# Kernel tuning notes

Measured on AMD Instinct MI355X. Metric: run time of the kernel, lower is better.

Reference implementation:

```python
import jax, jax.numpy as jnp
import numpy as np

TOTAL_TOKENS = 1_000_000   # total ragged flat values
EMB = 128                  # embedding_size
BATCH = 8192               # number of ragged rows (segments)


def setup_inputs() -> dict:
    key = jax.random.key(0)
    k1, k2, k3, k4, k5 = jax.random.split(key, 5)
    value = jax.random.normal(k1, (TOTAL_TOKENS, EMB), dtype=jnp.float32)
    key_emb = jax.random.normal(k2, (TOTAL_TOKENS, EMB), dtype=jnp.float32)
    segment_ids = jnp.sort(jax.random.randint(k3, (TOTAL_TOKENS,), 0, BATCH))
    fingerprint = jax.random.normal(k4, (EMB,), dtype=jnp.float32)
    w = jax.random.normal(k5, (EMB, EMB), dtype=jnp.float32) * 0.05
    return {"value": value, "key_emb": key_emb, "segment_ids": segment_ids,
            "fingerprint": fingerprint, "w": w}


def reference(value, key_emb, segment_ids, fingerprint, w):
    # Ragged branch: scores[i] = sum_k key[i,k] * w[k,k] * fingerprint[k]
    scale = jnp.sqrt(jnp.asarray(EMB, jnp.float32))
    diag_wf = jnp.diagonal(w) * fingerprint          # [E]
    scores = (key_emb @ diag_wf) / scale             # [T]
    # segment-wise (per ragged row) softmax
    smax = jax.ops.segment_max(scores, segment_ids, num_segments=BATCH)  # [B]
    ex = jnp.exp(scores - smax[segment_ids])                              # [T]
    denom = jax.ops.segment_sum(ex, segment_ids, num_segments=BATCH)     # [B]
    wts = ex / denom[segment_ids]                                         # [T]
    # weighted sum of concat([value, key], -1) over each ragged row
    feats = jnp.concatenate([value, key_emb], axis=-1)                    # [T, 2E]
    out = jax.ops.segment_sum(wts[:, None] * feats, segment_ids,
                              num_segments=BATCH)                         # [B, 2E]
    return out
```

## Files before the change

kernel.cpp:

```cpp
#include <hip/hip_runtime.h>
#include <cstdint>
#include <math.h>

#define EMB 128
#define CHUNK 64

__global__ void seg_starts_kernel(const int* __restrict__ seg, int T, int B,
                                  int* __restrict__ starts) {
    int b = blockIdx.x * blockDim.x + threadIdx.x;
    if (b > B) return;
    int lo = 0, hi = T;
    while (lo < hi) {
        int mid = (lo + hi) >> 1;
        if (seg[mid] < b) lo = mid + 1; else hi = mid;
    }
    starts[b] = lo;
}

__global__ __launch_bounds__(256, 4) void attn_kernel(
    const float* __restrict__ value, const float* __restrict__ key,
    const int* __restrict__ starts, const float* __restrict__ fingerprint,
    const float* __restrict__ w, float* __restrict__ out)
{
    __shared__ float key_lds[CHUNK * EMB];
    __shared__ float s_lds[CHUNK];
    __shared__ float e_lds[CHUNK];
    __shared__ float dwf_lds[EMB];
    __shared__ float red2[2];

    const int b   = blockIdx.x;
    const int tid = threadIdx.x;
    const int s0  = starts[b];
    const int s1  = starts[b + 1];
    const int len = s1 - s0;

    if (tid < EMB)
        dwf_lds[tid] = w[tid * EMB + tid] * fingerprint[tid] * 0.08838834764831845f;
    __syncthreads();

    const int lane = tid & 63;
    const int wv   = tid >> 6;
    const float dlo = dwf_lds[lane];
    const float dhi = dwf_lds[lane + 64];

    float acc   = 0.0f;
    float m     = -INFINITY;
    float denom = 0.0f;

    for (int o = 0; o < len; o += CHUNK) {
        const int cl = min(CHUNK, len - o);

        const float4* kbase = (const float4*)(key + (size_t)(s0 + o) * EMB);
        const int n4 = cl * (EMB / 4);
        for (int f = tid; f < n4; f += 256)
            ((float4*)key_lds)[f] = kbase[f];
        __syncthreads();

        for (int r = 0; r < CHUNK / 4; ++r) {
            int t = wv + 4 * r;
            if (t < cl) {
                float sc = key_lds[t * EMB + lane] * dlo
                         + key_lds[t * EMB + lane + 64] * dhi;
                #pragma unroll
                for (int off = 32; off; off >>= 1) sc += __shfl_xor(sc, off);
                if (lane == 0) s_lds[t] = sc;
            } else {
                if (lane == 0) s_lds[t] = -INFINITY;
            }
        }
        __syncthreads();

        const float m_old = m;
        if (wv == 0) {
            float s  = s_lds[lane];
            float mx = s;
            #pragma unroll
            for (int off = 32; off; off >>= 1) mx = fmaxf(mx, __shfl_xor(mx, off));
            float m_new = fmaxf(m_old, mx);
            float e = (s > -INFINITY) ? __expf(s - m_new) : 0.0f;
            e_lds[lane] = e;
            float ss = e;
            #pragma unroll
            for (int off = 32; off; off >>= 1) ss += __shfl_xor(ss, off);
            if (lane == 0) { red2[0] = m_new; red2[1] = ss; }
        }
        __syncthreads();
        const float m_new = red2[0];
        const float csum  = red2[1];
        const float alpha = (m_old > -INFINITY) ? __expf(m_old - m_new) : 0.0f;
        acc   = acc * alpha;
        denom = denom * alpha + csum;
        m     = m_new;

        if (tid < 128) {
            const float* vcol = value + (size_t)(s0 + o) * EMB + tid;
            #pragma unroll 4
            for (int t = 0; t < cl; ++t)
                acc = fmaf(e_lds[t], vcol[(size_t)t * EMB], acc);
        } else {
            const float* kcol = key_lds + (tid - 128);
            #pragma unroll 4
            for (int t = 0; t < cl; ++t)
                acc = fmaf(e_lds[t], kcol[t * EMB], acc);
        }
        __syncthreads();
    }

    const float r = (denom > 0.0f) ? acc / denom : 0.0f;
    out[(size_t)b * (2 * EMB) + tid] = r;
}

extern "C" void kernel_launch(void* const* d_in, const int* in_sizes, int n_in,
                              void* d_out, int out_size, void* d_ws, size_t ws_size,
                              hipStream_t stream) {
    const float* value = (const float*)d_in[0];
    const float* key   = (const float*)d_in[1];
    const int*   seg   = (const int*)d_in[2];
    const float* fp    = (const float*)d_in[3];
    const float* w     = (const float*)d_in[4];
    float* out = (float*)d_out;

    const int T = in_sizes[2];
    const int B = out_size / (2 * EMB);

    int* starts = (int*)d_ws;

    const int nb = (B + 1 + 255) / 256;
    seg_starts_kernel<<<nb, 256, 0, stream>>>(seg, T, B, starts);
    attn_kernel<<<B, 256, 0, stream>>>(value, key, starts, fp, w, out);
}
```

Before: 1.066 ms.

## Use direct global-to-LDS key loads with swizzle and vectorized row-parallel accumulation

Key chunks now go straight from global memory into LDS through global_load_lds, laid out with an XOR swizzle, and the chunk size drops to 32 with a higher occupancy hint. Scoring runs 8 lanes per row over float4 reads, every wave computes the softmax redundantly so one barrier and the shared e buffer go away, and the weighted sum is spread across waves and row halves as float4 accumulators. A final cross-wave reduction through LDS replaces the old per-column serial loops. The aim is to remove strided scalar global value loads and LDS bank conflicts. In exchange the kernel does more chunk iterations and a final reduction step, and clamped indices read extra rows whose weight is zero.

```diff
diff --git a/kernel.cpp b/kernel.cpp
--- a/kernel.cpp
+++ b/kernel.cpp
@@ -3,7 +3,7 @@
 #include <math.h>
 
 #define EMB 128
-#define CHUNK 64
+#define CHUNK 32
 
 __global__ void seg_starts_kernel(const int* __restrict__ seg, int T, int B,
                                   int* __restrict__ starts) {
@@ -17,19 +17,20 @@
     starts[b] = lo;
 }
 
-__global__ __launch_bounds__(256, 4) void attn_kernel(
+__global__ __launch_bounds__(256, 6) void attn_kernel(
     const float* __restrict__ value, const float* __restrict__ key,
     const int* __restrict__ starts, const float* __restrict__ fingerprint,
-    const float* __restrict__ w, float* __restrict__ out)
+    const float* __restrict__ w, float* __restrict__ out, int T)
 {
-    __shared__ float key_lds[CHUNK * EMB];
+    __shared__ __align__(16) float key_lds[CHUNK * EMB];
     __shared__ float s_lds[CHUNK];
-    __shared__ float e_lds[CHUNK];
-    __shared__ float dwf_lds[EMB];
-    __shared__ float red2[2];
+    __shared__ __align__(16) float dwf_lds[EMB];
 
-    const int b   = blockIdx.x;
-    const int tid = threadIdx.x;
+    const int b    = blockIdx.x;
+    const int tid  = threadIdx.x;
+    const int lane = tid & 63;
+    const int wv   = tid >> 6;
+
     const int s0  = starts[b];
     const int s1  = starts[b + 1];
     const int len = s1 - s0;
@@ -38,75 +39,116 @@
         dwf_lds[tid] = w[tid * EMB + tid] * fingerprint[tid] * 0.08838834764831845f;
     __syncthreads();
 
-    const int lane = tid & 63;
-    const int wv   = tid >> 6;
-    const float dlo = dwf_lds[lane];
-    const float dhi = dwf_lds[lane + 64];
+    const int g8   = lane >> 3;
+    const int j8   = lane & 7;
+    const int half = lane >> 5;
+    const int c4   = lane & 31;
 
-    float acc   = 0.0f;
-    float m     = -INFINITY;
-    float denom = 0.0f;
+    float4 dw[4];
+    #pragma unroll
+    for (int q = 0; q < 4; ++q)
+        dw[q] = *reinterpret_cast<const float4*>(&dwf_lds[j8 * 16 + q * 4]);
+
+    float4 vacc = make_float4(0.f, 0.f, 0.f, 0.f);
+    float4 kacc = make_float4(0.f, 0.f, 0.f, 0.f);
+    float m = -INFINITY, denom = 0.0f;
+
+    const char* key_b = (const char*)key;
 
     for (int o = 0; o < len; o += CHUNK) {
         const int cl = min(CHUNK, len - o);
 
-        const float4* kbase = (const float4*)(key + (size_t)(s0 + o) * EMB);
-        const int n4 = cl * (EMB / 4);
-        for (int f = tid; f < n4; f += 256)
-            ((float4*)key_lds)[f] = kbase[f];
-        __syncthreads();
-
-        for (int r = 0; r < CHUNK / 4; ++r) {
-            int t = wv + 4 * r;
-            if (t < cl) {
-                float sc = key_lds[t * EMB + lane] * dlo
-                         + key_lds[t * EMB + lane + 64] * dhi;
-                #pragma unroll
-                for (int off = 32; off; off >>= 1) sc += __shfl_xor(sc, off);
-                if (lane == 0) s_lds[t] = sc;
-            } else {
-                if (lane == 0) s_lds[t] = -INFINITY;
-            }
+        #pragma unroll
+        for (int i = 0; i < 4; ++i) {
+            const int q  = (wv << 2) + i;
+            const int r  = (q << 1) + half;
+            const int gr = min(s0 + o + r, T - 1);
+            const char* src = key_b + (size_t)gr * 512 + ((c4 ^ (r & 7)) << 4);
+            __builtin_amdgcn_global_load_lds(
+                (const __attribute__((address_space(1))) void*)src,
+                (__attribute__((address_space(3))) void*)(key_lds + (q << 8)),
+                16, 0, 0);
         }
         __syncthreads();
 
-        const float m_old = m;
-        if (wv == 0) {
-            float s  = s_lds[lane];
-            float mx = s;
-            #pragma unroll
-            for (int off = 32; off; off >>= 1) mx = fmaxf(mx, __shfl_xor(mx, off));
-            float m_new = fmaxf(m_old, mx);
-            float e = (s > -INFINITY) ? __expf(s - m_new) : 0.0f;
-            e_lds[lane] = e;
-            float ss = e;
-            #pragma unroll
-            for (int off = 32; off; off >>= 1) ss += __shfl_xor(ss, off);
-            if (lane == 0) { red2[0] = m_new; red2[1] = ss; }
+        {
+            const int t = (wv << 3) + g8;
+            float sc = 0.0f;
+            if (t < cl) {
+                const char* rowp = (const char*)key_lds + t * 512;
+                const int swz = (t & 7) << 4;
+                #pragma unroll
+                for (int q = 0; q < 4; ++q) {
+                    const float4 k = *reinterpret_cast<const float4*>(
+                        rowp + (((((j8 << 2) + q) << 4)) ^ swz));
+                    sc = fmaf(k.x, dw[q].x, sc);
+                    sc = fmaf(k.y, dw[q].y, sc);
+                    sc = fmaf(k.z, dw[q].z, sc);
+                    sc = fmaf(k.w, dw[q].w, sc);
+                }
+            }
+            sc += __shfl_xor(sc, 1);
+            sc += __shfl_xor(sc, 2);
+            sc += __shfl_xor(sc, 4);
+            if (j8 == 0) s_lds[t] = (t < cl) ? sc : -INFINITY;
         }
         __syncthreads();
-        const float m_new = red2[0];
-        const float csum  = red2[1];
-        const float alpha = (m_old > -INFINITY) ? __expf(m_old - m_new) : 0.0f;
-        acc   = acc * alpha;
-        denom = denom * alpha + csum;
-        m     = m_new;
 
-        if (tid < 128) {
-            const float* vcol = value + (size_t)(s0 + o) * EMB + tid;
-            #pragma unroll 4
-            for (int t = 0; t < cl; ++t)
-                acc = fmaf(e_lds[t], vcol[(size_t)t * EMB], acc);
-        } else {
-            const float* kcol = key_lds + (tid - 128);
-            #pragma unroll 4
-            for (int t = 0; t < cl; ++t)
-                acc = fmaf(e_lds[t], kcol[t * EMB], acc);
+        const float s = (lane < CHUNK) ? s_lds[lane] : -INFINITY;
+        float mx = s;
+        #pragma unroll
+        for (int off = 32; off; off >>= 1) mx = fmaxf(mx, __shfl_xor(mx, off));
+        const float m_new = fmaxf(m, mx);
+        const float e = (s > -INFINITY) ? __expf(s - m_new) : 0.0f;
+        float cs = e;
+        #pragma unroll
+        for (int off = 32; off; off >>= 1) cs += __shfl_xor(cs, off);
+        const float alpha = (m > -INFINITY) ? __expf(m - m_new) : 0.0f;
+        denom = denom * alpha + cs;
+        m = m_new;
+        vacc.x *= alpha; vacc.y *= alpha; vacc.z *= alpha; vacc.w *= alpha;
+        kacc.x *= alpha; kacc.y *= alpha; kacc.z *= alpha; kacc.w *= alpha;
+
+        const float4* vrow4 = (const float4*)(value + (size_t)(s0 + o) * EMB);
+        #pragma unroll
+        for (int pp = 0; pp < 4; ++pp) {
+            const int t  = ((wv + (pp << 2)) << 1) + half;
+            const int tc = min(t, cl - 1);
+            const float et = __shfl(e, t);
+            const float4 v = vrow4[(size_t)tc * 32 + c4];
+            const float4 kk = *reinterpret_cast<const float4*>(
+                (const char*)key_lds + tc * 512 + ((c4 ^ (tc & 7)) << 4));
+            vacc.x = fmaf(et, v.x, vacc.x);
+            vacc.y = fmaf(et, v.y, vacc.y);
+            vacc.z = fmaf(et, v.z, vacc.z);
+            vacc.w = fmaf(et, v.w, vacc.w);
+            kacc.x = fmaf(et, kk.x, kacc.x);
+            kacc.y = fmaf(et, kk.y, kacc.y);
+            kacc.z = fmaf(et, kk.z, kacc.z);
+            kacc.w = fmaf(et, kk.w, kacc.w);
         }
         __syncthreads();
     }
 
-    const float r = (denom > 0.0f) ? acc / denom : 0.0f;
+    vacc.x += __shfl_xor(vacc.x, 32);
+    vacc.y += __shfl_xor(vacc.y, 32);
+    vacc.z += __shfl_xor(vacc.z, 32);
+    vacc.w += __shfl_xor(vacc.w, 32);
+    kacc.x += __shfl_xor(kacc.x, 32);
+    kacc.y += __shfl_xor(kacc.y, 32);
+    kacc.z += __shfl_xor(kacc.z, 32);
+    kacc.w += __shfl_xor(kacc.w, 32);
+
+    if (lane < 32) {
+        float4* dst = reinterpret_cast<float4*>(key_lds);
+        dst[(wv << 6) + c4]      = vacc;
+        dst[(wv << 6) + 32 + c4] = kacc;
+    }
+    __syncthreads();
+
+    const float sum = key_lds[tid] + key_lds[256 + tid]
+                    + key_lds[512 + tid] + key_lds[768 + tid];
+    const float r = (denom > 0.0f) ? sum / denom : 0.0f;
     out[(size_t)b * (2 * EMB) + tid] = r;
 }
 
@@ -127,5 +169,5 @@
 
     const int nb = (B + 1 + 255) / 256;
     seg_starts_kernel<<<nb, 256, 0, stream>>>(seg, T, B, starts);
-    attn_kernel<<<B, 256, 0, stream>>>(value, key, starts, fp, w, out);
+    attn_kernel<<<B, 256, 0, stream>>>(value, key, starts, fp, w, out, T);
 }
```

Measured after the change: 1.002 ms. -6.0%, faster.
